# Optimization experiments

Measured on AMD Instinct MI355X. Metric: run time of the kernel, lower is better.

## Reference

```python
import jax, jax.numpy as jnp
import numpy as np

# Grid constants from point_cloud_range and PILLAR_SIZE (KITTI PointPillars defaults)
PX, PY, PZ = 0.16, 0.16, 4.0
X0, Y0, Z0 = 0.0, -39.68, -3.0
NX, NY, NZ = 432, 496, 1
X_OFF = PX / 2 + X0
Y_OFF = PY / 2 + Y0
Z_OFF = PZ / 2 + Z0
B = 8          # batch size
P = 96000      # total pillars across batch
M = 32         # max points per pillar
CIN = 10       # 4 base + 3 cluster + 3 center
COUT = 64      # FILTERS[-1]
BN_EPS = 1e-3


def setup_inputs() -> dict:
    key = jax.random.key(0)
    k1, k2, k3, k4, k5, k6 = jax.random.split(key, 6)
    pillars = jax.random.normal(k1, (P, M, 4), dtype=jnp.float32)
    b = jax.random.randint(k2, (P,), 0, B, dtype=jnp.int32)
    z = jnp.zeros((P,), dtype=jnp.int32)  # nz == 1
    y = jax.random.randint(k3, (P,), 0, NY, dtype=jnp.int32)
    x = jax.random.randint(k4, (P,), 0, NX, dtype=jnp.int32)
    coords = jnp.stack([b, z, y, x], axis=1)  # (P, 4) as [batch, z, y, x]
    num_points = jax.random.randint(k5, (P,), 1, M + 1, dtype=jnp.int32)
    W = jax.random.normal(k6, (CIN, COUT), dtype=jnp.float32) * 0.05
    gamma = jnp.ones((COUT,), dtype=jnp.float32)
    beta = jnp.zeros((COUT,), dtype=jnp.float32)
    return {"pillars": pillars, "coords": coords, "num_points": num_points,
            "W": W, "gamma": gamma, "beta": beta}


def _pfe_forward(pillars, W, gamma, beta, coords, num_points):
    # --- feature augmentation ---
    abs_xyz = pillars[:, :, :3]                                   # (P, M, 3)
    n = num_points.astype(pillars.dtype)[:, None, None]
    mean_xyz = jnp.sum(abs_xyz, axis=1, keepdims=True) / n        # (P, 1, 3)
    xyz_to_cluster = abs_xyz - mean_xyz                           # (P, M, 3)
    cz = coords[:, 1].astype(pillars.dtype)
    cy = coords[:, 2].astype(pillars.dtype)
    cx = coords[:, 3].astype(pillars.dtype)
    centers = jnp.stack([cx * PX + X_OFF, cy * PY + Y_OFF, cz * PZ + Z_OFF], axis=-1)
    xyz_to_center = abs_xyz - centers[:, None, :]                 # (P, M, 3)
    feats = jnp.concatenate([pillars, xyz_to_cluster, xyz_to_center], axis=-1)  # (P, M, 10)

    # --- PFNLayer: linear (no bias) + BatchNorm1d (train-mode batch stats) + ReLU + max over points ---
    h = jnp.einsum("pmi,io->pmo", feats, W)                       # (P, M, COUT)
    mu = jnp.mean(h, axis=(0, 1))
    var = jnp.var(h, axis=(0, 1))                                 # biased, like torch BN
    h = (h - mu) * jax.lax.rsqrt(var + BN_EPS) * gamma + beta
    h = jax.nn.relu(h)
    pv = jnp.max(h, axis=1)                                       # (P, COUT)

    # --- scatter pillar features to dense BEV grid ---
    cell = coords[:, 1] + coords[:, 2] * NX + coords[:, 3]        # z + y*nx + x
    flat = coords[:, 0] * (NZ * NY * NX) + cell                   # (P,)
    bev = jnp.zeros((B * NZ * NY * NX, COUT), dtype=pv.dtype).at[flat].set(pv)
    bev = bev.reshape(B, NZ * NY * NX, COUT).transpose(0, 2, 1)   # (B, C, nz*ny*nx)
    return bev.reshape(B, COUT * NZ, NY, NX)


def reference(pillars, coords, num_points, W, gamma, beta):
    return _pfe_forward(pillars, W, gamma, beta, coords, num_points)
```

## Files before the change

### kernel.cpp

```cpp
#include <hip/hip_runtime.h>

#define NPILLARS 96000
#define MPTS 32
#define NCHAN 64
#define NXC 432
#define NYC 496
#define NB 8
#define NCELLS (NXC*NYC)
#define NBLK 1024
#define PXc 0.16f
#define PYc 0.16f
#define PZc 4.0f
#define XOFF (0.08f)
#define YOFF (0.08f - 39.68f)
#define ZOFF (2.0f - 3.0f)
#define BN_EPS 1e-3f

typedef __attribute__((ext_vector_type(8))) short short8;
typedef __attribute__((ext_vector_type(16))) float float16;

__device__ __forceinline__ short f2bf(float x) {
    union { float f; unsigned u; } v; v.f = x;
    unsigned r = v.u + 0x7FFFu + ((v.u >> 16) & 1u);
    return (short)(r >> 16);
}

#define PAIRS(Q) \
 Q(0,0,0) Q(1,0,1) Q(2,0,2) Q(3,0,3) Q(4,0,4) Q(5,0,5) Q(6,0,6) Q(7,0,7) Q(8,0,8) Q(9,0,9) \
 Q(10,1,1) Q(11,1,2) Q(12,1,3) Q(13,1,4) Q(14,1,5) Q(15,1,6) Q(16,1,7) Q(17,1,8) Q(18,1,9) \
 Q(19,2,2) Q(20,2,3) Q(21,2,4) Q(22,2,5) Q(23,2,6) Q(24,2,7) Q(25,2,8) Q(26,2,9) \
 Q(27,3,3) Q(28,3,4) Q(29,3,5) Q(30,3,6) Q(31,3,7) Q(32,3,8) Q(33,3,9) \
 Q(34,4,4) Q(35,4,5) Q(36,4,6) Q(37,4,7) Q(38,4,8) Q(39,4,9) \
 Q(40,5,5) Q(41,5,6) Q(42,5,7) Q(43,5,8) Q(44,5,9) \
 Q(45,6,6) Q(46,6,7) Q(47,6,8) Q(48,6,9) \
 Q(49,7,7) Q(50,7,8) Q(51,7,9) \
 Q(52,8,8) Q(53,8,9) \
 Q(54,9,9)

__global__ __launch_bounds__(256, 4)
void k_moments(const float4* __restrict__ pillars,
               const int* __restrict__ coords,
               const int* __restrict__ num_points,
               float* __restrict__ partial,
               int* __restrict__ winner) {
    const int tid  = threadIdx.x;
    const int lane = tid & 63;
    const int sub  = lane & 31;
    const int half = lane >> 5;
    const int wv   = tid >> 6;
    const int wid    = (blockIdx.x * blockDim.x + tid) >> 6;
    const int nwaves = (gridDim.x * blockDim.x) >> 6;

    float s0=0.f,s1=0.f,s2=0.f,s3=0.f,s4=0.f,s5=0.f,s6=0.f,s7=0.f,s8=0.f,s9=0.f;
#define QDECL(idx,i,j) float q_##i##_##j = 0.f;
    PAIRS(QDECL)
#undef QDECL

    for (int base = wid * 2; base < NPILLARS; base += nwaves * 2) {
        const int p = base + half;
        float4 pt = pillars[p * MPTS + sub];
        float sx = pt.x, sy = pt.y, sz = pt.z;
#pragma unroll
        for (int m = 16; m >= 1; m >>= 1) {
            sx += __shfl_xor(sx, m);
            sy += __shfl_xor(sy, m);
            sz += __shfl_xor(sz, m);
        }
        const float n = (float)num_points[p];
        const float mx = sx / n, my = sy / n, mz = sz / n;
        const int   cb  = coords[p*4+0];
        const int   czi = coords[p*4+1], cyi = coords[p*4+2], cxi = coords[p*4+3];
        const float ctx = (float)cxi * PXc + XOFF;
        const float cty = (float)cyi * PYc + YOFF;
        const float ctz = (float)czi * PZc + ZOFF;
        const float f0=pt.x, f1=pt.y, f2=pt.z, f3=pt.w;
        const float f4=pt.x-mx,  f5=pt.y-my,  f6=pt.z-mz;
        const float f7=pt.x-ctx, f8=pt.y-cty, f9=pt.z-ctz;
        s0+=f0; s1+=f1; s2+=f2; s3+=f3; s4+=f4;
        s5+=f5; s6+=f6; s7+=f7; s8+=f8; s9+=f9;
#define QACC(idx,i,j) q_##i##_##j = fmaf(f##i, f##j, q_##i##_##j);
        PAIRS(QACC)
#undef QACC
        if (sub == 0) {
            const int cell = czi + cyi * NXC + cxi;
            atomicMax(&winner[cb * NCELLS + cell], p);
        }
    }

    __shared__ float lds_part[4][65];
#define RED6(v) { v += __shfl_xor(v,32); v += __shfl_xor(v,16); v += __shfl_xor(v,8); \
                  v += __shfl_xor(v,4);  v += __shfl_xor(v,2);  v += __shfl_xor(v,1); }
    RED6(s0) RED6(s1) RED6(s2) RED6(s3) RED6(s4)
    RED6(s5) RED6(s6) RED6(s7) RED6(s8) RED6(s9)
#define QRED(idx,i,j) RED6(q_##i##_##j)
    PAIRS(QRED)
#undef QRED
#undef RED6
    if (lane == 0) {
        float* dst = &lds_part[wv][0];
        dst[0]=s0; dst[1]=s1; dst[2]=s2; dst[3]=s3; dst[4]=s4;
        dst[5]=s5; dst[6]=s6; dst[7]=s7; dst[8]=s8; dst[9]=s9;
#define QST(idx,i,j) dst[10+idx] = q_##i##_##j;
        PAIRS(QST)
#undef QST
    }
    __syncthreads();
    if (tid < 65) {
        const float acc = lds_part[0][tid] + lds_part[1][tid]
                        + lds_part[2][tid] + lds_part[3][tid];
        partial[tid * NBLK + blockIdx.x] = acc;
    }
}

__global__ void k_finalize(const float* __restrict__ partial,
                           const float* __restrict__ W,
                           const float* __restrict__ gamma,
                           const float* __restrict__ beta,
                           float* __restrict__ ss) {
    __shared__ float mom[65];
    for (int i = threadIdx.x; i < 65; i += blockDim.x) {
        const float4* p4 = (const float4*)(partial + (size_t)i * NBLK);
        float a0=0.f, a1=0.f, a2=0.f, a3=0.f;
        for (int b = 0; b < NBLK/4; b++) {
            float4 v = p4[b];
            a0 += v.x; a1 += v.y; a2 += v.z; a3 += v.w;
        }
        mom[i] = (a0 + a1) + (a2 + a3);
    }
    __syncthreads();
    const int c = threadIdx.x;
    if (c >= 64) return;
    const double invN = 1.0 / ((double)NPILLARS * (double)MPTS);
    double wv[10];
#pragma unroll
    for (int i = 0; i < 10; i++) wv[i] = (double)W[i * NCHAN + c];
    double mu = 0.0;
#pragma unroll
    for (int i = 0; i < 10; i++) mu += (double)mom[i] * wv[i];
    mu *= invN;
    double e2 = 0.0;
#define QFOLD(idx,i,j) { double t = (double)mom[10+idx] * wv[i] * wv[j]; \
                         e2 += (i == j) ? t : 2.0 * t; }
    PAIRS(QFOLD)
#undef QFOLD
    e2 *= invN;
    const double var = e2 - mu * mu;
    const float scale = (float)((double)gamma[c] / sqrt(var + (double)BN_EPS));
    const float shift = beta[c] - (float)mu * scale;
    ss[c] = scale;
    ss[64 + c] = shift;
}

__global__ __launch_bounds__(256, 4)
void k_pv(const float4* __restrict__ pillars,
          const int* __restrict__ coords,
          const int* __restrict__ num_points,
          const float* __restrict__ W,
          const float* __restrict__ ss,
          float* __restrict__ pv) {
    const int tid  = threadIdx.x;
    const int lane = tid & 63;
    const int sub  = lane & 31;
    const int half = lane >> 5;
    const int wid    = (blockIdx.x * blockDim.x + tid) >> 6;
    const int nwaves = (gridDim.x * blockDim.x) >> 6;

    short8 bf0, bf1;
#pragma unroll
    for (int r = 0; r < 8; r++) {
        const int k = half * 8 + r;
        bf0[r] = (k < 10) ? f2bf(W[k * NCHAN + sub])      : (short)0;
        bf1[r] = (k < 10) ? f2bf(W[k * NCHAN + 32 + sub]) : (short)0;
    }
    const float scale0 = ss[sub],      shift0 = ss[64 + sub];
    const float scale1 = ss[32 + sub], shift1 = ss[96 + sub];

    for (int p = wid; p < NPILLARS; p += nwaves) {
        float4 pt = pillars[p * MPTS + sub];
        float sx = pt.x, sy = pt.y, sz = pt.z;
#pragma unroll
        for (int m = 16; m >= 1; m >>= 1) {
            sx += __shfl_xor(sx, m);
            sy += __shfl_xor(sy, m);
            sz += __shfl_xor(sz, m);
        }
        const float n = (float)num_points[p];
        const float mx = sx / n, my = sy / n, mz = sz / n;
        const float ctx = (float)coords[p*4+3] * PXc + XOFF;
        const float cty = (float)coords[p*4+2] * PYc + YOFF;
        const float ctz = (float)coords[p*4+1] * PZc + ZOFF;
        const short b0 = f2bf(pt.x),     b1 = f2bf(pt.y),     b2 = f2bf(pt.z),
                    b3 = f2bf(pt.w),     b4 = f2bf(pt.x-mx),  b5 = f2bf(pt.y-my),
                    b6 = f2bf(pt.z-mz),  b7 = f2bf(pt.x-ctx), b8 = f2bf(pt.y-cty),
                    b9 = f2bf(pt.z-ctz);
        short8 a;
        a[0] = half ? b8 : b0;
        a[1] = half ? b9 : b1;
        a[2] = half ? (short)0 : b2;
        a[3] = half ? (short)0 : b3;
        a[4] = half ? (short)0 : b4;
        a[5] = half ? (short)0 : b5;
        a[6] = half ? (short)0 : b6;
        a[7] = half ? (short)0 : b7;
        float16 acc0 = {};
        float16 acc1 = {};
        acc0 = __builtin_amdgcn_mfma_f32_32x32x16_bf16(a, bf0, acc0, 0, 0, 0);
        acc1 = __builtin_amdgcn_mfma_f32_32x32x16_bf16(a, bf1, acc1, 0, 0, 0);
        float m0 = 0.f, m1 = 0.f;
#pragma unroll
        for (int r = 0; r < 16; r++) {
            m0 = fmaxf(m0, fmaf(acc0[r], scale0, shift0));
            m1 = fmaxf(m1, fmaf(acc1[r], scale1, shift1));
        }
        m0 = fmaxf(m0, __shfl_xor(m0, 32));
        m1 = fmaxf(m1, __shfl_xor(m1, 32));
        pv[p * NCHAN + lane] = half ? m1 : m0;
    }
}

__global__ void k_expand(const int* __restrict__ winner,
                         const float* __restrict__ pv,
                         float* __restrict__ out) {
    const int idx = blockIdx.x * blockDim.x + threadIdx.x;
    const int total4 = NB * NCELLS / 4;
    if (idx >= total4) return;
    const int b    = (idx << 2) / NCELLS;
    const int cell = (idx << 2) - b * NCELLS;
    const int4 w = ((const int4*)winner)[idx];
    float* obase = out + (size_t)b * NCHAN * NCELLS + cell;
#pragma unroll 4
    for (int c = 0; c < NCHAN; c++) {
        float4 v;
        v.x = (w.x >= 0) ? pv[w.x * NCHAN + c] : 0.f;
        v.y = (w.y >= 0) ? pv[w.y * NCHAN + c] : 0.f;
        v.z = (w.z >= 0) ? pv[w.z * NCHAN + c] : 0.f;
        v.w = (w.w >= 0) ? pv[w.w * NCHAN + c] : 0.f;
        *reinterpret_cast<float4*>(obase + (size_t)c * NCELLS) = v;
    }
}

extern "C" void kernel_launch(void* const* d_in, const int* in_sizes, int n_in,
                              void* d_out, int out_size, void* d_ws, size_t ws_size,
                              hipStream_t stream) {
    const float4* pillars    = (const float4*)d_in[0];
    const int*    coords     = (const int*)d_in[1];
    const int*    num_points = (const int*)d_in[2];
    const float*  W          = (const float*)d_in[3];
    const float*  gamma      = (const float*)d_in[4];
    const float*  beta       = (const float*)d_in[5];
    float* out = (float*)d_out;

    char* ws = (char*)d_ws;
    float* ss     = (float*)ws;
    int*   winner = (int*)(ws + 4096);
    float* pv     = (float*)(ws + 4096 + (size_t)NB * NCELLS * sizeof(int));
    float* partial = pv;

    hipMemsetAsync(winner, 0xFF, (size_t)NB * NCELLS * sizeof(int), stream);

    k_moments <<<NBLK, 256, 0, stream>>>(pillars, coords, num_points, partial, winner);
    k_finalize<<<1, 256, 0, stream>>>(partial, W, gamma, beta, ss);
    k_pv      <<<2048, 256, 0, stream>>>(pillars, coords, num_points, W, ss, pv);
    k_expand  <<<(NB * NCELLS / 4 + 255) / 256, 256, 0, stream>>>(winner, pv, out);
}
```

Before: 580.0 us.

## Vectorize coord loads, parallelize finalize, widen expand with nontemporal stores

Coordinates are now read as a single int4 per pillar instead of four scalar loads. The finalize reduction spreads work over 260 threads, each summing a quarter of one moment row, and combines the pieces with shared-memory atomics instead of 65 serial threads. The expand kernel now handles 8 cells per thread and writes the output with nontemporal stores, which is meant to cut cache pollution on the large BEV write. These are several independent small changes. Float atomic ordering changes the summation order slightly, and the wider expand gives fewer threads for latency hiding.

```diff
diff --git a/kernel.cpp b/kernel.cpp
--- a/kernel.cpp
+++ b/kernel.cpp
@@ -18,6 +18,7 @@
 
 typedef __attribute__((ext_vector_type(8))) short short8;
 typedef __attribute__((ext_vector_type(16))) float float16;
+typedef __attribute__((ext_vector_type(4))) float natf4;
 
 __device__ __forceinline__ short f2bf(float x) {
     union { float f; unsigned u; } v; v.f = x;
@@ -39,7 +40,7 @@
 
 __global__ __launch_bounds__(256, 4)
 void k_moments(const float4* __restrict__ pillars,
-               const int* __restrict__ coords,
+               const int4* __restrict__ coords,
                const int* __restrict__ num_points,
                float* __restrict__ partial,
                int* __restrict__ winner) {
@@ -68,11 +69,10 @@
         }
         const float n = (float)num_points[p];
         const float mx = sx / n, my = sy / n, mz = sz / n;
-        const int   cb  = coords[p*4+0];
-        const int   czi = coords[p*4+1], cyi = coords[p*4+2], cxi = coords[p*4+3];
-        const float ctx = (float)cxi * PXc + XOFF;
-        const float cty = (float)cyi * PYc + YOFF;
-        const float ctz = (float)czi * PZc + ZOFF;
+        const int4  cd = coords[p];
+        const float ctx = (float)cd.w * PXc + XOFF;
+        const float cty = (float)cd.z * PYc + YOFF;
+        const float ctz = (float)cd.y * PZc + ZOFF;
         const float f0=pt.x, f1=pt.y, f2=pt.z, f3=pt.w;
         const float f4=pt.x-mx,  f5=pt.y-my,  f6=pt.z-mz;
         const float f7=pt.x-ctx, f8=pt.y-cty, f9=pt.z-ctz;
@@ -82,8 +82,8 @@
         PAIRS(QACC)
 #undef QACC
         if (sub == 0) {
-            const int cell = czi + cyi * NXC + cxi;
-            atomicMax(&winner[cb * NCELLS + cell], p);
+            const int cell = cd.y + cd.z * NXC + cd.w;
+            atomicMax(&winner[cd.x * NCELLS + cell], p);
         }
     }
 
@@ -118,17 +118,22 @@
                            const float* __restrict__ beta,
                            float* __restrict__ ss) {
     __shared__ float mom[65];
-    for (int i = threadIdx.x; i < 65; i += blockDim.x) {
-        const float4* p4 = (const float4*)(partial + (size_t)i * NBLK);
+    const int tid = threadIdx.x;
+    if (tid < 65) mom[tid] = 0.f;
+    __syncthreads();
+    for (int task = tid; task < 65 * 4; task += 256) {
+        const int i = task >> 2, ch = task & 3;
+        const float4* p4 = (const float4*)(partial + (size_t)i * NBLK) + ch * (NBLK/16);
         float a0=0.f, a1=0.f, a2=0.f, a3=0.f;
-        for (int b = 0; b < NBLK/4; b++) {
+#pragma unroll 8
+        for (int b = 0; b < NBLK/16; b++) {
             float4 v = p4[b];
             a0 += v.x; a1 += v.y; a2 += v.z; a3 += v.w;
         }
-        mom[i] = (a0 + a1) + (a2 + a3);
+        atomicAdd(&mom[i], (a0 + a1) + (a2 + a3));
     }
     __syncthreads();
-    const int c = threadIdx.x;
+    const int c = tid;
     if (c >= 64) return;
     const double invN = 1.0 / ((double)NPILLARS * (double)MPTS);
     double wv[10];
@@ -153,7 +158,7 @@
 
 __global__ __launch_bounds__(256, 4)
 void k_pv(const float4* __restrict__ pillars,
-          const int* __restrict__ coords,
+          const int4* __restrict__ coords,
           const int* __restrict__ num_points,
           const float* __restrict__ W,
           const float* __restrict__ ss,
@@ -186,9 +191,10 @@
         }
         const float n = (float)num_points[p];
         const float mx = sx / n, my = sy / n, mz = sz / n;
-        const float ctx = (float)coords[p*4+3] * PXc + XOFF;
-        const float cty = (float)coords[p*4+2] * PYc + YOFF;
-        const float ctz = (float)coords[p*4+1] * PZc + ZOFF;
+        const int4  cd = coords[p];
+        const float ctx = (float)cd.w * PXc + XOFF;
+        const float cty = (float)cd.z * PYc + YOFF;
+        const float ctz = (float)cd.y * PZc + ZOFF;
         const short b0 = f2bf(pt.x),     b1 = f2bf(pt.y),     b2 = f2bf(pt.z),
                     b3 = f2bf(pt.w),     b4 = f2bf(pt.x-mx),  b5 = f2bf(pt.y-my),
                     b6 = f2bf(pt.z-mz),  b7 = f2bf(pt.x-ctx), b8 = f2bf(pt.y-cty),
@@ -222,20 +228,27 @@
                          const float* __restrict__ pv,
                          float* __restrict__ out) {
     const int idx = blockIdx.x * blockDim.x + threadIdx.x;
-    const int total4 = NB * NCELLS / 4;
-    if (idx >= total4) return;
-    const int b    = (idx << 2) / NCELLS;
-    const int cell = (idx << 2) - b * NCELLS;
-    const int4 w = ((const int4*)winner)[idx];
+    const int total8 = NB * NCELLS / 8;
+    if (idx >= total8) return;
+    const int b    = (idx << 3) / NCELLS;
+    const int cell = (idx << 3) - b * NCELLS;
+    const int4 w0 = ((const int4*)winner)[idx * 2];
+    const int4 w1 = ((const int4*)winner)[idx * 2 + 1];
     float* obase = out + (size_t)b * NCHAN * NCELLS + cell;
 #pragma unroll 4
     for (int c = 0; c < NCHAN; c++) {
-        float4 v;
-        v.x = (w.x >= 0) ? pv[w.x * NCHAN + c] : 0.f;
-        v.y = (w.y >= 0) ? pv[w.y * NCHAN + c] : 0.f;
-        v.z = (w.z >= 0) ? pv[w.z * NCHAN + c] : 0.f;
-        v.w = (w.w >= 0) ? pv[w.w * NCHAN + c] : 0.f;
-        *reinterpret_cast<float4*>(obase + (size_t)c * NCELLS) = v;
+        natf4 v0, v1;
+        v0.x = (w0.x >= 0) ? pv[w0.x * NCHAN + c] : 0.f;
+        v0.y = (w0.y >= 0) ? pv[w0.y * NCHAN + c] : 0.f;
+        v0.z = (w0.z >= 0) ? pv[w0.z * NCHAN + c] : 0.f;
+        v0.w = (w0.w >= 0) ? pv[w0.w * NCHAN + c] : 0.f;
+        v1.x = (w1.x >= 0) ? pv[w1.x * NCHAN + c] : 0.f;
+        v1.y = (w1.y >= 0) ? pv[w1.y * NCHAN + c] : 0.f;
+        v1.z = (w1.z >= 0) ? pv[w1.z * NCHAN + c] : 0.f;
+        v1.w = (w1.w >= 0) ? pv[w1.w * NCHAN + c] : 0.f;
+        natf4* o = reinterpret_cast<natf4*>(obase + (size_t)c * NCELLS);
+        __builtin_nontemporal_store(v0, o);
+        __builtin_nontemporal_store(v1, o + 1);
     }
 }
 
@@ -243,7 +256,7 @@
                               void* d_out, int out_size, void* d_ws, size_t ws_size,
                               hipStream_t stream) {
     const float4* pillars    = (const float4*)d_in[0];
-    const int*    coords     = (const int*)d_in[1];
+    const int4*   coords     = (const int4*)d_in[1];
     const int*    num_points = (const int*)d_in[2];
     const float*  W          = (const float*)d_in[3];
     const float*  gamma      = (const float*)d_in[4];
@@ -256,10 +269,10 @@
     float* pv     = (float*)(ws + 4096 + (size_t)NB * NCELLS * sizeof(int));
     float* partial = pv;
 
-    hipMemsetAsync(winner, 0xFF, (size_t)NB * NCELLS * sizeof(int), stream);
+    (void)hipMemsetAsync(winner, 0xFF, (size_t)NB * NCELLS * sizeof(int), stream);
 
     k_moments <<<NBLK, 256, 0, stream>>>(pillars, coords, num_points, partial, winner);
     k_finalize<<<1, 256, 0, stream>>>(partial, W, gamma, beta, ss);
     k_pv      <<<2048, 256, 0, stream>>>(pillars, coords, num_points, W, ss, pv);
-    k_expand  <<<(NB * NCELLS / 4 + 255) / 256, 256, 0, stream>>>(winner, pv, out);
-}
+    k_expand  <<<(NB * NCELLS / 8 + 255) / 256, 256, 0, stream>>>(winner, pv, out);
+}
```

After: 654.8 us. 1.13x slower.
